# Performance work log

Measured on AMD Instinct MI355X. Metric: run time of the kernel, lower is better.

## Reference

```python
import jax, jax.numpy as jnp
import numpy as np

L, N, C = 1024, 32, 512
EPS = 1e-5

def _linear(y, W, b):
    # torch nn.Linear: y @ W.T + b ; y: (L,N,C), W: (C,C)
    return jnp.einsum('lnc,dc->lnd', y, W) + b

def _bn(y, gamma, beta):
    # training-mode BatchNorm1d over (N, C, L) -> stats per channel over (L, N)
    m = y.mean(axis=(0, 1))
    v = y.var(axis=(0, 1))  # biased variance, as torch uses for normalization
    return (y - m) * jax.lax.rsqrt(v + EPS) * gamma + beta

def _indrnn(y, u):
    # h_t = relu(x_t + u * h_{t-1}), elementwise per-channel recurrence over L
    h0 = jnp.zeros(y.shape[1:], y.dtype)
    def step(h, xt):
        h = jax.nn.relu(xt + u * h)
        return h, h
    _, hs = jax.lax.scan(step, h0, y)
    return hs

def setup_inputs() -> dict:
    key = jax.random.key(0)
    ks = jax.random.split(key, 12)
    s = 1.0 / np.sqrt(C)
    x = jax.random.normal(ks[0], (L, N, C), dtype=jnp.float32)
    W1 = jax.random.uniform(ks[1], (C, C), jnp.float32, -s, s)
    b1 = jax.random.uniform(ks[2], (C,), jnp.float32, -s, s)
    g1 = jnp.ones((C,), jnp.float32)
    be1 = jnp.zeros((C,), jnp.float32)
    u1 = jax.random.uniform(ks[3], (C,), jnp.float32, 0.0, 1.0)
    W2 = jax.random.uniform(ks[4], (C, C), jnp.float32, -s, s)
    b2 = jax.random.uniform(ks[5], (C,), jnp.float32, -s, s)
    g2 = jnp.ones((C,), jnp.float32)
    be2 = jnp.zeros((C,), jnp.float32)
    u2 = jax.random.uniform(ks[6], (C,), jnp.float32, 0.0, 1.0)
    return {"x": x, "W1": W1, "b1": b1, "g1": g1, "be1": be1, "u1": u1,
            "W2": W2, "b2": b2, "g2": g2, "be2": be2, "u2": u2}

def reference(x, W1, b1, g1, be1, u1, W2, b2, g2, be2, u2):
    # linear_first=True branch; dropout=0.0 -> identity
    y = _linear(x, W1, b1)
    y = _bn(y, g1, be1)
    y = _indrnn(y, u1)
    y = _linear(y, W2, b2)
    y = _bn(y, g2, be2)
    y = _indrnn(y, u2)
    return y + x
```

## Files before the change

kernel.cpp:

```cpp
#include <hip/hip_runtime.h>
#include <stdint.h>

#define L_DIM 1024
#define N_DIM 32
#define C_DIM 512
#define M_DIM (L_DIM * N_DIM)
#define EPS_BN 1e-5f

typedef __attribute__((ext_vector_type(8))) short bf16x8;
typedef __attribute__((ext_vector_type(4))) float f32x4;

__device__ __forceinline__ unsigned short f2bf(float f) {
  union { float f; unsigned int u; } a; a.f = f;
  unsigned int u = a.u;
  return (unsigned short)((u + 0x7FFFu + ((u >> 16) & 1u)) >> 16);
}
__device__ __forceinline__ float bf2f(unsigned short h) {
  union { float f; unsigned int u; } a; a.u = ((unsigned int)h) << 16;
  return a.f;
}

__device__ __forceinline__ void gl16(const void* g, void* l) {
  __builtin_amdgcn_global_load_lds(
      (const __attribute__((address_space(1))) unsigned int*)g,
      (__attribute__((address_space(3))) unsigned int*)l, 16, 0, 0);
}

__global__ void k_split_all(const float* __restrict__ x, const float* __restrict__ W1,
                            const float* __restrict__ W2,
                            unsigned short* __restrict__ Ahi,
                            unsigned short* __restrict__ W1hi,
                            unsigned short* __restrict__ W2hi) {
  const int NX = M_DIM * C_DIM / 4;
  const int NW = C_DIM * C_DIM / 4;
  int i = blockIdx.x * 256 + threadIdx.x;
  int stride = gridDim.x * 256;
  for (; i < NX + 2 * NW; i += stride) {
    const float4* src; unsigned short* dh; int j;
    if (i < NX)            { src = (const float4*)x;  dh = Ahi;  j = i; }
    else if (i < NX + NW)  { src = (const float4*)W1; dh = W1hi; j = i - NX; }
    else                   { src = (const float4*)W2; dh = W2hi; j = i - NX - NW; }
    float4 v = src[j];
    ushort4 h;
    h.x = f2bf(v.x); h.y = f2bf(v.y); h.z = f2bf(v.z); h.w = f2bf(v.w);
    ((ushort4*)dh)[j] = h;
  }
}

__global__ __launch_bounds__(256, 2)
void k_gemm(const unsigned short* __restrict__ A,
            const unsigned short* __restrict__ B,
            const float* __restrict__ bias, unsigned short* __restrict__ C,
            float* __restrict__ gsum, float* __restrict__ gsq) {
  const int K = C_DIM;
  int d = blockIdx.x;
  int xcd = d & 7;
  int q = d >> 3;
  int bm = xcd * 32 + (q >> 2);
  int bn = q & 3;

  __shared__ unsigned short lds[2][16384];

  int tid  = threadIdx.x;
  int lane = tid & 63;
  int wave = tid >> 6;
  int wm = wave >> 1;
  int wn = wave & 1;
  int lr = lane & 15;
  int lk = lane >> 4;

  f32x4 acc[4][4];
#pragma unroll
  for (int i = 0; i < 4; ++i)
#pragma unroll
    for (int j = 0; j < 4; ++j) acc[i][j] = (f32x4){0.f, 0.f, 0.f, 0.f};

  const int r0 = tid & 127;
  const int kc0 = tid >> 7;
  const int oa0 = (bm * 128 + r0) * K + (kc0 + 0) * 8;
  const int oa1 = (bm * 128 + r0) * K + (kc0 + 2) * 8;
  const int oa2 = (bm * 128 + r0) * K + (kc0 + 4) * 8;
  const int oa3 = (bm * 128 + r0) * K + (kc0 + 6) * 8;
  const int ob0 = (bn * 128 + r0) * K + (kc0 + 0) * 8;
  const int ob1 = (bn * 128 + r0) * K + (kc0 + 2) * 8;
  const int ob2 = (bn * 128 + r0) * K + (kc0 + 4) * 8;
  const int ob3 = (bn * 128 + r0) * K + (kc0 + 6) * 8;

#define STAGE(buf, kk)                                          \
  do {                                                          \
    unsigned short* Lb = lds[buf];                              \
    gl16(A + oa0 + (kk), Lb + (tid) * 8);                       \
    gl16(A + oa1 + (kk), Lb + (tid + 256) * 8);                 \
    gl16(A + oa2 + (kk), Lb + (tid + 512) * 8);                 \
    gl16(A + oa3 + (kk), Lb + (tid + 768) * 8);                 \
    gl16(B + ob0 + (kk), Lb + (tid + 1024) * 8);                \
    gl16(B + ob1 + (kk), Lb + (tid + 1280) * 8);                \
    gl16(B + ob2 + (kk), Lb + (tid + 1536) * 8);                \
    gl16(B + ob3 + (kk), Lb + (tid + 1792) * 8);                \
  } while (0)

#define COMPUTE(buf)                                                          \
  do {                                                                        \
    const unsigned short* Lb = lds[buf];                                      \
    _Pragma("unroll")                                                         \
    for (int kc2 = 0; kc2 < 2; ++kc2) {                                       \
      bf16x8 bh[4], af[4];                                                    \
      _Pragma("unroll")                                                       \
      for (int nj = 0; nj < 4; ++nj) {                                        \
        int slot = 1024 + (kc2 * 4 + lk) * 128 + wn * 64 + nj * 16 + lr;      \
        bh[nj] = *(const bf16x8*)(Lb + slot * 8);                             \
      }                                                                       \
      _Pragma("unroll")                                                       \
      for (int mi = 0; mi < 4; ++mi) {                                        \
        int slot = (kc2 * 4 + lk) * 128 + wm * 64 + mi * 16 + lr;             \
        af[mi] = *(const bf16x8*)(Lb + slot * 8);                             \
      }                                                                       \
      _Pragma("unroll")                                                       \
      for (int mi = 0; mi < 4; ++mi)                                          \
        _Pragma("unroll")                                                     \
        for (int nj = 0; nj < 4; ++nj)                                        \
          acc[mi][nj] = __builtin_amdgcn_mfma_f32_16x16x32_bf16(af[mi], bh[nj], acc[mi][nj], 0, 0, 0); \
    }                                                                         \
  } while (0)

  const int nt = K >> 6;
  STAGE(0, 0);
  STAGE(1, 64);

  for (int t = 0; t < nt - 1; ++t) {
    asm volatile("s_waitcnt vmcnt(8)" ::: "memory");
    __builtin_amdgcn_sched_barrier(0);
    __builtin_amdgcn_s_barrier();
    COMPUTE(t & 1);
    __builtin_amdgcn_s_barrier();
    if (t < nt - 2) STAGE(t & 1, (t + 2) << 6);
  }
  asm volatile("s_waitcnt vmcnt(0)" ::: "memory");
  __builtin_amdgcn_sched_barrier(0);
  __builtin_amdgcn_s_barrier();
  COMPUTE((nt - 1) & 1);

  __syncthreads();
  float* T = (float*)&lds[0][0];
#pragma unroll
  for (int nj = 0; nj < 4; ++nj) {
    int gn = bn * 128 + wn * 64 + nj * 16 + lr;
    float bv = bias[gn];
    float s = 0.f, qq = 0.f;
    int lcol = wn * 64 + nj * 16 + lr;
#pragma unroll
    for (int mi = 0; mi < 4; ++mi) {
      int lrow = wm * 64 + mi * 16 + (lk << 2);
#pragma unroll
      for (int r = 0; r < 4; ++r) {
        float v = acc[mi][nj][r] + bv;
        T[(lrow + r) * 128 + lcol] = v;
        s += v; qq += v * v;
      }
    }
    s  += __shfl_xor(s, 16);  qq += __shfl_xor(qq, 16);
    s  += __shfl_xor(s, 32);  qq += __shfl_xor(qq, 32);
    if (lk == 0) {
      atomicAdd(&gsum[gn], s);
      atomicAdd(&gsq[gn], qq);
    }
  }
  __syncthreads();
  {
    int rr = tid >> 4, jj = tid & 15;
#pragma unroll
    for (int i = 0; i < 8; ++i) {
      int row = i * 16 + rr;
      const float* src = T + row * 128 + jj * 8;
      f32x4 a0 = *(const f32x4*)src;
      f32x4 a1 = *(const f32x4*)(src + 4);
      union { unsigned int u[4]; bf16x8 v; } P;
      P.u[0] = (unsigned int)f2bf(a0[0]) | ((unsigned int)f2bf(a0[1]) << 16);
      P.u[1] = (unsigned int)f2bf(a0[2]) | ((unsigned int)f2bf(a0[3]) << 16);
      P.u[2] = (unsigned int)f2bf(a1[0]) | ((unsigned int)f2bf(a1[1]) << 16);
      P.u[3] = (unsigned int)f2bf(a1[2]) | ((unsigned int)f2bf(a1[3]) << 16);
      *(bf16x8*)(C + (size_t)(bm * 128 + row) * C_DIM + bn * 128 + jj * 8) = P.v;
    }
  }
#undef STAGE
#undef COMPUTE
}


__global__ __launch_bounds__(1024, 4)
void k_indrnn_split(const unsigned short* __restrict__ y,
                    const float* __restrict__ gsum, const float* __restrict__ gsq,
                    const float* __restrict__ g, const float* __restrict__ be,
                    const float* __restrict__ u,
                    unsigned short* __restrict__ hhi) {
  __shared__ float tA[1024], tB[1024], tM[1024];
  int lane = threadIdx.x & 63;
  int w = threadIdx.x >> 6;
  int chain = blockIdx.x * 64 + lane;
  int c = chain & 511;
  float m  = gsum[c] * (1.0f / (float)M_DIM);
  float vv = gsq[c]  * (1.0f / (float)M_DIM) - m * m;
  float sc = g[c] * rsqrtf(vv + EPS_BN);
  float sh = be[c] - m * sc;
  float uu = u[c];
  const unsigned short* py = y + chain;
  const int base = w * 64;

  float A = 0.f, Bc = 1.f, Mx = 0.f;
  for (int c0 = 0; c0 < 64; c0 += 16) {
    float vb[16];
#pragma unroll
    for (int i = 0; i < 16; ++i) vb[i] = bf2f(py[(base + c0 + i) * 16384]);
#pragma unroll
    for (int i = 0; i < 16; ++i) {
      float xt = fmaf(vb[i], sc, sh);
      A  = fmaf(uu, A, xt);
      Mx = fmaxf(fmaf(uu, Mx, xt), 0.f);
      Bc *= uu;
    }
  }
  tA[w * 64 + lane] = A; tB[w * 64 + lane] = Bc; tM[w * 64 + lane] = Mx;
  __syncthreads();

  float pA = 0.f, pM = 0.f;
  for (int s = 0; s < w; ++s) {
    float a = tA[s * 64 + lane], b = tB[s * 64 + lane], mm = tM[s * 64 + lane];
    pA = fmaf(b, pA, a);
    pM = fmaxf(fmaf(b, pM, a), mm);
  }
  float h = fmaxf(pA, pM);

  unsigned short* ph = hhi + chain;
  for (int c0 = 0; c0 < 64; c0 += 16) {
    float vb[16];
#pragma unroll
    for (int i = 0; i < 16; ++i) vb[i] = bf2f(py[(base + c0 + i) * 16384]);
#pragma unroll
    for (int i = 0; i < 16; ++i) {
      float xt = fmaf(vb[i], sc, sh);
      h = fmaxf(fmaf(uu, h, xt), 0.f);
      ph[(base + c0 + i) * 16384] = f2bf(h);
    }
  }
}

__global__ __launch_bounds__(1024, 4)
void k_indrnn_res(const unsigned short* __restrict__ y, const float* __restrict__ x,
                  float* __restrict__ outp,
                  const float* __restrict__ gsum, const float* __restrict__ gsq,
                  const float* __restrict__ g, const float* __restrict__ be,
                  const float* __restrict__ u) {
  __shared__ float tA[1024], tB[1024], tM[1024];
  int lane = threadIdx.x & 63;
  int w = threadIdx.x >> 6;
  int chain = blockIdx.x * 64 + lane;
  int c = chain & 511;
  float m  = gsum[c] * (1.0f / (float)M_DIM);
  float vv = gsq[c]  * (1.0f / (float)M_DIM) - m * m;
  float sc = g[c] * rsqrtf(vv + EPS_BN);
  float sh = be[c] - m * sc;
  float uu = u[c];
  const unsigned short* py = y + chain;
  const float* px = x + chain;
  float* po = outp + chain;
  const int base = w * 64;

  float A = 0.f, Bc = 1.f, Mx = 0.f;
  for (int c0 = 0; c0 < 64; c0 += 16) {
    float vb[16];
#pragma unroll
    for (int i = 0; i < 16; ++i) vb[i] = bf2f(py[(base + c0 + i) * 16384]);
#pragma unroll
    for (int i = 0; i < 16; ++i) {
      float xt = fmaf(vb[i], sc, sh);
      A  = fmaf(uu, A, xt);
      Mx = fmaxf(fmaf(uu, Mx, xt), 0.f);
      Bc *= uu;
    }
  }
  tA[w * 64 + lane] = A; tB[w * 64 + lane] = Bc; tM[w * 64 + lane] = Mx;
  __syncthreads();

  float pA = 0.f, pM = 0.f;
  for (int s = 0; s < w; ++s) {
    float a = tA[s * 64 + lane], b = tB[s * 64 + lane], mm = tM[s * 64 + lane];
    pA = fmaf(b, pA, a);
    pM = fmaxf(fmaf(b, pM, a), mm);
  }
  float h = fmaxf(pA, pM);

  for (int c0 = 0; c0 < 64; c0 += 16) {
    float vb[16], xb[16];
#pragma unroll
    for (int i = 0; i < 16; ++i) vb[i] = bf2f(py[(base + c0 + i) * 16384]);
#pragma unroll
    for (int i = 0; i < 16; ++i) xb[i] = px[(base + c0 + i) * 16384];
#pragma unroll
    for (int i = 0; i < 16; ++i) {
      float xt = fmaf(vb[i], sc, sh);
      h = fmaxf(fmaf(uu, h, xt), 0.f);
      po[(base + c0 + i) * 16384] = h + xb[i];
    }
  }
}

extern "C" void kernel_launch(void* const* d_in, const int* in_sizes, int n_in,
                              void* d_out, int out_size, void* d_ws, size_t ws_size,
                              hipStream_t stream) {
  if (n_in < 11) return;
  const float* x   = (const float*)d_in[0];
  const float* W1  = (const float*)d_in[1];
  const float* b1  = (const float*)d_in[2];
  const float* g1  = (const float*)d_in[3];
  const float* be1 = (const float*)d_in[4];
  const float* u1  = (const float*)d_in[5];
  const float* W2  = (const float*)d_in[6];
  const float* b2  = (const float*)d_in[7];
  const float* g2  = (const float*)d_in[8];
  const float* be2 = (const float*)d_in[9];
  const float* u2  = (const float*)d_in[10];
  float* out = (float*)d_out;

  char* ws = (char*)d_ws;
  const size_t SZ_HALF = (size_t)M_DIM * C_DIM * sizeof(unsigned short);
  const size_t SZ_W    = (size_t)C_DIM * C_DIM * sizeof(unsigned short);
  unsigned short* Ahi  = (unsigned short*)(ws);
  unsigned short* Cbf  = (unsigned short*)(ws + SZ_HALF);
  unsigned short* W1hi = (unsigned short*)(ws + 2 * SZ_HALF);
  unsigned short* W2hi = W1hi + C_DIM * C_DIM;
  float* stats = (float*)(ws + 2 * SZ_HALF + 2 * SZ_W);
  float* sum1 = stats,        *sq1 = stats + 512;
  float* sum2 = stats + 1024, *sq2 = stats + 1536;
  if (ws_size < 2 * SZ_HALF + 2 * SZ_W + 4 * 512 * sizeof(float)) return;

  hipMemsetAsync(stats, 0, 4 * 512 * sizeof(float), stream);

  k_split_all<<<2048, 256, 0, stream>>>(x, W1, W2, Ahi, W1hi, W2hi);

  dim3 gemmGrid(1024);
  k_gemm<<<gemmGrid, 256, 0, stream>>>(Ahi, W1hi, b1, Cbf, sum1, sq1);
  k_indrnn_split<<<256, 1024, 0, stream>>>(Cbf, sum1, sq1, g1, be1, u1, Ahi);

  k_gemm<<<gemmGrid, 256, 0, stream>>>(Ahi, W2hi, b2, Cbf, sum2, sq2);
  k_indrnn_res<<<256, 1024, 0, stream>>>(Cbf, x, out, sum2, sq2, g2, be2, u2);
}
```

Before: 152.3 us.

## Replace direct global-to-LDS loads with register-staged double-buffered GEMM pipeline

The GEMM main loop no longer uses global_load_lds to fill LDS. Each tile is loaded into registers, written to the alternate LDS buffer, and computed on in a fully unrolled schedule with one barrier per round. The aim is to overlap global latency with MFMA work and drop one barrier per iteration. The cost is more VGPR pressure from two register staging sets, and the loop is hardcoded for K=512 (eight tiles).

```diff
diff --git a/kernel.cpp b/kernel.cpp
--- a/kernel.cpp
+++ b/kernel.cpp
@@ -18,12 +18,6 @@
 __device__ __forceinline__ float bf2f(unsigned short h) {
   union { float f; unsigned int u; } a; a.u = ((unsigned int)h) << 16;
   return a.f;
-}
-
-__device__ __forceinline__ void gl16(const void* g, void* l) {
-  __builtin_amdgcn_global_load_lds(
-      (const __attribute__((address_space(1))) unsigned int*)g,
-      (__attribute__((address_space(3))) unsigned int*)l, 16, 0, 0);
 }
 
 __global__ void k_split_all(const float* __restrict__ x, const float* __restrict__ W1,
@@ -86,18 +80,61 @@
   const int ob2 = (bn * 128 + r0) * K + (kc0 + 4) * 8;
   const int ob3 = (bn * 128 + r0) * K + (kc0 + 6) * 8;
 
-#define STAGE(buf, kk)                                          \
-  do {                                                          \
-    unsigned short* Lb = lds[buf];                              \
-    gl16(A + oa0 + (kk), Lb + (tid) * 8);                       \
-    gl16(A + oa1 + (kk), Lb + (tid + 256) * 8);                 \
-    gl16(A + oa2 + (kk), Lb + (tid + 512) * 8);                 \
-    gl16(A + oa3 + (kk), Lb + (tid + 768) * 8);                 \
-    gl16(B + ob0 + (kk), Lb + (tid + 1024) * 8);                \
-    gl16(B + ob1 + (kk), Lb + (tid + 1280) * 8);                \
-    gl16(B + ob2 + (kk), Lb + (tid + 1536) * 8);                \
-    gl16(B + ob3 + (kk), Lb + (tid + 1792) * 8);                \
-  } while (0)
+  bf16x8 rA0, rA1, rA2, rA3, rB0, rB1, rB2, rB3;
+  bf16x8 sA0, sA1, sA2, sA3, sB0, sB1, sB2, sB3;
+
+#define LOADE(kk)                                   \
+  do {                                              \
+    rA0 = *(const bf16x8*)(A + oa0 + (kk));         \
+    rA1 = *(const bf16x8*)(A + oa1 + (kk));         \
+    rA2 = *(const bf16x8*)(A + oa2 + (kk));         \
+    rA3 = *(const bf16x8*)(A + oa3 + (kk));         \
+    rB0 = *(const bf16x8*)(B + ob0 + (kk));         \
+    rB1 = *(const bf16x8*)(B + ob1 + (kk));         \
+    rB2 = *(const bf16x8*)(B + ob2 + (kk));         \
+    rB3 = *(const bf16x8*)(B + ob3 + (kk));         \
+  } while (0)
+#define LOADO(kk)                                   \
+  do {                                              \
+    sA0 = *(const bf16x8*)(A + oa0 + (kk));         \
+    sA1 = *(const bf16x8*)(A + oa1 + (kk));         \
+    sA2 = *(const bf16x8*)(A + oa2 + (kk));         \
+    sA3 = *(const bf16x8*)(A + oa3 + (kk));         \
+    sB0 = *(const bf16x8*)(B + ob0 + (kk));         \
+    sB1 = *(const bf16x8*)(B + ob1 + (kk));         \
+    sB2 = *(const bf16x8*)(B + ob2 + (kk));         \
+    sB3 = *(const bf16x8*)(B + ob3 + (kk));         \
+  } while (0)
+#define WRITEE(buf)                                 \
+  do {                                              \
+    unsigned short* Lb = lds[buf];                  \
+    *(bf16x8*)(Lb + (tid) * 8)        = rA0;        \
+    *(bf16x8*)(Lb + (tid + 256) * 8)  = rA1;        \
+    *(bf16x8*)(Lb + (tid + 512) * 8)  = rA2;        \
+    *(bf16x8*)(Lb + (tid + 768) * 8)  = rA3;        \
+    *(bf16x8*)(Lb + (tid + 1024) * 8) = rB0;        \
+    *(bf16x8*)(Lb + (tid + 1280) * 8) = rB1;        \
+    *(bf16x8*)(Lb + (tid + 1536) * 8) = rB2;        \
+    *(bf16x8*)(Lb + (tid + 1792) * 8) = rB3;        \
+  } while (0)
+#define WRITEO(buf)                                 \
+  do {                                              \
+    unsigned short* Lb = lds[buf];                  \
+    *(bf16x8*)(Lb + (tid) * 8)        = sA0;        \
+    *(bf16x8*)(Lb + (tid + 256) * 8)  = sA1;        \
+    *(bf16x8*)(Lb + (tid + 512) * 8)  = sA2;        \
+    *(bf16x8*)(Lb + (tid + 768) * 8)  = sA3;        \
+    *(bf16x8*)(Lb + (tid + 1024) * 8) = sB0;        \
+    *(bf16x8*)(Lb + (tid + 1280) * 8) = sB1;        \
+    *(bf16x8*)(Lb + (tid + 1536) * 8) = sB2;        \
+    *(bf16x8*)(Lb + (tid + 1792) * 8) = sB3;        \
+  } while (0)
+
+#define ROUND_BAR()                                          \
+    asm volatile("s_waitcnt lgkmcnt(0)" ::: "memory");       \
+    __builtin_amdgcn_sched_barrier(0);                       \
+    __builtin_amdgcn_s_barrier();                            \
+    __builtin_amdgcn_sched_barrier(0)
 
 #define COMPUTE(buf)                                                          \
   do {                                                                        \
@@ -123,22 +160,26 @@
     }                                                                         \
   } while (0)
 
-  const int nt = K >> 6;
-  STAGE(0, 0);
-  STAGE(1, 64);
-
-  for (int t = 0; t < nt - 1; ++t) {
-    asm volatile("s_waitcnt vmcnt(8)" ::: "memory");
-    __builtin_amdgcn_sched_barrier(0);
-    __builtin_amdgcn_s_barrier();
-    COMPUTE(t & 1);
-    __builtin_amdgcn_s_barrier();
-    if (t < nt - 2) STAGE(t & 1, (t + 2) << 6);
-  }
-  asm volatile("s_waitcnt vmcnt(0)" ::: "memory");
-  __builtin_amdgcn_sched_barrier(0);
-  __builtin_amdgcn_s_barrier();
-  COMPUTE((nt - 1) & 1);
+  LOADE(0);
+  LOADO(64);
+  WRITEE(0);
+  ROUND_BAR();
+#pragma unroll
+  for (int tt = 0; tt < 3; ++tt) {
+    int t0 = tt * 2;
+    LOADE((t0 + 2) << 6);
+    WRITEO(1);
+    COMPUTE(0);
+    ROUND_BAR();
+    LOADO((t0 + 3) << 6);
+    WRITEE(0);
+    COMPUTE(1);
+    ROUND_BAR();
+  }
+  WRITEO(1);
+  COMPUTE(0);
+  ROUND_BAR();
+  COMPUTE(1);
 
   __syncthreads();
   float* T = (float*)&lds[0][0];
@@ -182,7 +223,11 @@
       *(bf16x8*)(C + (size_t)(bm * 128 + row) * C_DIM + bn * 128 + jj * 8) = P.v;
     }
   }
-#undef STAGE
+#undef LOADE
+#undef LOADO
+#undef WRITEE
+#undef WRITEO
+#undef ROUND_BAR
 #undef COMPUTE
 }
 
```

Measured after the change: 154.6 us. About the same (+1.5%).

## Load GEMM MFMA fragments directly from global memory, bypassing LDS staging

Applied to the files above, without the earlier changes.

Replaces the double-buffered global_load_lds staging plus LDS fragment reads with per-wave direct global loads of bf16x8 fragments into registers, software-pipelined in two register sets across the K loop. This removes LDS traffic and the block barriers inside the main loop. In exchange, each fragment is fetched from global/L2 by both waves that share it instead of once per block, and it raises register pressure. Global loads are 16 bytes per lane with a row stride of 1 KB, so coalescing is poor.

```diff
diff --git a/kernel.cpp b/kernel.cpp
--- a/kernel.cpp
+++ b/kernel.cpp
@@ -18,12 +18,6 @@
 __device__ __forceinline__ float bf2f(unsigned short h) {
   union { float f; unsigned int u; } a; a.u = ((unsigned int)h) << 16;
   return a.f;
-}
-
-__device__ __forceinline__ void gl16(const void* g, void* l) {
-  __builtin_amdgcn_global_load_lds(
-      (const __attribute__((address_space(1))) unsigned int*)g,
-      (__attribute__((address_space(3))) unsigned int*)l, 16, 0, 0);
 }
 
 __global__ void k_split_all(const float* __restrict__ x, const float* __restrict__ W1,
@@ -52,14 +46,13 @@
             const unsigned short* __restrict__ B,
             const float* __restrict__ bias, unsigned short* __restrict__ C,
             float* __restrict__ gsum, float* __restrict__ gsq) {
-  const int K = C_DIM;
   int d = blockIdx.x;
   int xcd = d & 7;
   int q = d >> 3;
   int bm = xcd * 32 + (q >> 2);
   int bn = q & 3;
 
-  __shared__ unsigned short lds[2][16384];
+  __shared__ float T[16384];
 
   int tid  = threadIdx.x;
   int lane = tid & 63;
@@ -75,73 +68,38 @@
 #pragma unroll
     for (int j = 0; j < 4; ++j) acc[i][j] = (f32x4){0.f, 0.f, 0.f, 0.f};
 
-  const int r0 = tid & 127;
-  const int kc0 = tid >> 7;
-  const int oa0 = (bm * 128 + r0) * K + (kc0 + 0) * 8;
-  const int oa1 = (bm * 128 + r0) * K + (kc0 + 2) * 8;
-  const int oa2 = (bm * 128 + r0) * K + (kc0 + 4) * 8;
-  const int oa3 = (bm * 128 + r0) * K + (kc0 + 6) * 8;
-  const int ob0 = (bn * 128 + r0) * K + (kc0 + 0) * 8;
-  const int ob1 = (bn * 128 + r0) * K + (kc0 + 2) * 8;
-  const int ob2 = (bn * 128 + r0) * K + (kc0 + 4) * 8;
-  const int ob3 = (bn * 128 + r0) * K + (kc0 + 6) * 8;
-
-#define STAGE(buf, kk)                                          \
-  do {                                                          \
-    unsigned short* Lb = lds[buf];                              \
-    gl16(A + oa0 + (kk), Lb + (tid) * 8);                       \
-    gl16(A + oa1 + (kk), Lb + (tid + 256) * 8);                 \
-    gl16(A + oa2 + (kk), Lb + (tid + 512) * 8);                 \
-    gl16(A + oa3 + (kk), Lb + (tid + 768) * 8);                 \
-    gl16(B + ob0 + (kk), Lb + (tid + 1024) * 8);                \
-    gl16(B + ob1 + (kk), Lb + (tid + 1280) * 8);                \
-    gl16(B + ob2 + (kk), Lb + (tid + 1536) * 8);                \
-    gl16(B + ob3 + (kk), Lb + (tid + 1792) * 8);                \
+  const unsigned short* pA = A + (size_t)(bm * 128 + wm * 64 + lr) * C_DIM + lk * 8;
+  const unsigned short* pB = B + (size_t)(bn * 128 + wn * 64 + lr) * C_DIM + lk * 8;
+
+#define LOADF(AF, BF, kk)                                         \
+  do {                                                            \
+    _Pragma("unroll")                                             \
+    for (int mi = 0; mi < 4; ++mi)                                \
+      AF[mi] = *(const bf16x8*)(pA + mi * 8192 + (kk));           \
+    _Pragma("unroll")                                             \
+    for (int nj = 0; nj < 4; ++nj)                                \
+      BF[nj] = *(const bf16x8*)(pB + nj * 8192 + (kk));           \
   } while (0)
 
-#define COMPUTE(buf)                                                          \
-  do {                                                                        \
-    const unsigned short* Lb = lds[buf];                                      \
-    _Pragma("unroll")                                                         \
-    for (int kc2 = 0; kc2 < 2; ++kc2) {                                       \
-      bf16x8 bh[4], af[4];                                                    \
-      _Pragma("unroll")                                                       \
-      for (int nj = 0; nj < 4; ++nj) {                                        \
-        int slot = 1024 + (kc2 * 4 + lk) * 128 + wn * 64 + nj * 16 + lr;      \
-        bh[nj] = *(const bf16x8*)(Lb + slot * 8);                             \
-      }                                                                       \
-      _Pragma("unroll")                                                       \
-      for (int mi = 0; mi < 4; ++mi) {                                        \
-        int slot = (kc2 * 4 + lk) * 128 + wm * 64 + mi * 16 + lr;             \
-        af[mi] = *(const bf16x8*)(Lb + slot * 8);                             \
-      }                                                                       \
-      _Pragma("unroll")                                                       \
-      for (int mi = 0; mi < 4; ++mi)                                          \
-        _Pragma("unroll")                                                     \
-        for (int nj = 0; nj < 4; ++nj)                                        \
-          acc[mi][nj] = __builtin_amdgcn_mfma_f32_16x16x32_bf16(af[mi], bh[nj], acc[mi][nj], 0, 0, 0); \
-    }                                                                         \
+#define MM(AF, BF)                                                \
+  do {                                                            \
+    _Pragma("unroll")                                             \
+    for (int mi = 0; mi < 4; ++mi)                                \
+      _Pragma("unroll")                                           \
+      for (int nj = 0; nj < 4; ++nj)                              \
+        acc[mi][nj] = __builtin_amdgcn_mfma_f32_16x16x32_bf16(AF[mi], BF[nj], acc[mi][nj], 0, 0, 0); \
   } while (0)
 
-  const int nt = K >> 6;
-  STAGE(0, 0);
-  STAGE(1, 64);
-
-  for (int t = 0; t < nt - 1; ++t) {
-    asm volatile("s_waitcnt vmcnt(8)" ::: "memory");
-    __builtin_amdgcn_sched_barrier(0);
-    __builtin_amdgcn_s_barrier();
-    COMPUTE(t & 1);
-    __builtin_amdgcn_s_barrier();
-    if (t < nt - 2) STAGE(t & 1, (t + 2) << 6);
-  }
-  asm volatile("s_waitcnt vmcnt(0)" ::: "memory");
-  __builtin_amdgcn_sched_barrier(0);
-  __builtin_amdgcn_s_barrier();
-  COMPUTE((nt - 1) & 1);
-
-  __syncthreads();
-  float* T = (float*)&lds[0][0];
+  bf16x8 aE[4], bE[4], aO[4], bO[4];
+  LOADF(aE, bE, 0);
+#pragma unroll
+  for (int s = 0; s < 16; s += 2) {
+    if (s + 1 < 16) LOADF(aO, bO, (s + 1) * 32);
+    MM(aE, bE);
+    if (s + 2 < 16) LOADF(aE, bE, (s + 2) * 32);
+    MM(aO, bO);
+  }
+
 #pragma unroll
   for (int nj = 0; nj < 4; ++nj) {
     int gn = bn * 128 + wn * 64 + nj * 16 + lr;
@@ -182,8 +140,8 @@
       *(bf16x8*)(C + (size_t)(bm * 128 + row) * C_DIM + bn * 128 + jj * 8) = P.v;
     }
   }
-#undef STAGE
-#undef COMPUTE
+#undef LOADF
+#undef MM
 }
 
 
```

Result: slower. 209.2 us (+37.3%).
